# Performance work log

Measured on AMD Instinct MI355X. Metric: run time of the kernel, lower is better.

The kernel has to match this reference:

```python
import jax, jax.numpy as jnp
import numpy as np

NUM_HEADS = 12


def _get_rel_pos(q_size, k_size, rel_pos):
    # q_size == k_size here, so the torch interpolate branch is never taken;
    # table already has 2*max(q,k)-1 rows. Gather by relative coordinate.
    coords = jnp.arange(q_size)[:, None] - jnp.arange(k_size)[None, :] + (k_size - 1)
    return rel_pos[coords]  # (q_size, k_size, head_dim)


def setup_inputs() -> dict:
    key = jax.random.key(0)
    ks = jax.random.split(key, 8)
    B, D, H, W, dim = 32, 8, 8, 8, 768
    hd = dim // NUM_HEADS
    s = 0.02
    return {
        "x": jax.random.normal(ks[0], (B, D, H, W, dim), jnp.float32),
        "w_qkv": jax.random.normal(ks[1], (dim, 3 * dim), jnp.float32) * s,
        "b_qkv": jnp.zeros((3 * dim,), jnp.float32),
        "w_proj": jax.random.normal(ks[2], (dim, dim), jnp.float32) * s,
        "b_proj": jnp.zeros((dim,), jnp.float32),
        "rel_pos_d": jax.random.normal(ks[3], (2 * D - 1, hd), jnp.float32) * s,
        "rel_pos_h": jax.random.normal(ks[4], (2 * H - 1, hd), jnp.float32) * s,
        "rel_pos_w": jax.random.normal(ks[5], (2 * W - 1, hd), jnp.float32) * s,
    }


def reference(x, w_qkv, b_qkv, w_proj, b_proj, rel_pos_d, rel_pos_h, rel_pos_w):
    B, D, H, W, dim = x.shape
    nH = NUM_HEADS
    hd = dim // nH
    N = D * H * W
    scale = hd ** -0.5

    # qkv projection: (B, N, 3, nH, hd) -> (3, B*nH, N, hd)
    qkv = (x.reshape(B, N, dim) @ w_qkv + b_qkv).reshape(B, N, 3, nH, hd)
    qkv = jnp.transpose(qkv, (2, 0, 3, 1, 4)).reshape(3, B * nH, N, hd)
    q, k, v = qkv[0], qkv[1], qkv[2]

    attn = jnp.einsum('bqc,bkc->bqk', q * scale, k)  # (B*nH, N, N)

    # decomposed relative positional bias (MViTv2-style)
    Rd = _get_rel_pos(D, D, rel_pos_d)  # (D, D, hd)
    Rh = _get_rel_pos(H, H, rel_pos_h)  # (H, H, hd)
    Rw = _get_rel_pos(W, W, rel_pos_w)  # (W, W, hd)
    r_q = q.reshape(B * nH, D, H, W, hd)
    rel_d = jnp.einsum('bdhwc,dkc->bdhwk', r_q, Rd)
    rel_h = jnp.einsum('bdhwc,hkc->bdhwk', r_q, Rh)
    rel_w = jnp.einsum('bdhwc,wkc->bdhwk', r_q, Rw)

    attn = attn.reshape(B * nH, D, H, W, D, H, W)
    attn = (attn
            + rel_d[:, :, :, :, :, None, None]
            + rel_h[:, :, :, :, None, :, None]
            + rel_w[:, :, :, :, None, None, :])
    attn = jax.nn.softmax(attn.reshape(B * nH, N, N), axis=-1)

    out = (attn @ v).reshape(B, nH, D, H, W, hd)
    out = jnp.transpose(out, (0, 2, 3, 4, 1, 5)).reshape(B, D, H, W, dim)
    return out @ w_proj + b_proj
```

## Files before the change

### kernel.cpp

```cpp
#include <hip/hip_runtime.h>
#include <hip/hip_bf16.h>
#include <cstdint>

typedef __bf16 bf16x8 __attribute__((ext_vector_type(8)));
typedef __bf16 bf16x4 __attribute__((ext_vector_type(4)));
typedef float  f32x4  __attribute__((ext_vector_type(4)));
typedef float  f32x16 __attribute__((ext_vector_type(16)));
typedef unsigned u32x4 __attribute__((ext_vector_type(4)));

__device__ __forceinline__ f32x4 mfma16(bf16x8 a, bf16x8 b, f32x4 c) {
  return __builtin_amdgcn_mfma_f32_16x16x32_bf16(a, b, c, 0, 0, 0);
}
__device__ __forceinline__ f32x16 mfma32(bf16x8 a, bf16x8 b, f32x16 c) {
  return __builtin_amdgcn_mfma_f32_32x32x16_bf16(a, b, c, 0, 0, 0);
}

__device__ __forceinline__ void gload_lds16(const __bf16* g, __bf16* l) {
  __builtin_amdgcn_global_load_lds(
      (const __attribute__((address_space(1))) void*)g,
      (__attribute__((address_space(3))) void*)l, 16, 0, 0);
}

__device__ __forceinline__ unsigned cvtpk(float lo, float hi) {
  unsigned r;
  asm("v_cvt_pk_bf16_f32 %0, %1, %2" : "=v"(r) : "v"(lo), "v"(hi));
  return r;
}
__device__ __forceinline__ void plswap(unsigned& a, unsigned& b) {
  asm("v_permlane32_swap_b32 %0, %1" : "+v"(a), "+v"(b));
}

__global__ __launch_bounds__(256) void cvt_bf16_kernel(const float* __restrict__ in,
                                                       __bf16* __restrict__ out, int n4) {
  int i = blockIdx.x * 256 + threadIdx.x;
  if (i < n4) {
    float4 v = ((const float4*)in)[i];
    bf16x4 o;
    o[0] = (__bf16)v.x; o[1] = (__bf16)v.y; o[2] = (__bf16)v.z; o[3] = (__bf16)v.w;
    ((bf16x4*)out)[i] = o;
  }
}

__global__ __launch_bounds__(256) void transpose_cvt_kernel(const float* __restrict__ src,
                                                            __bf16* __restrict__ dst,
                                                            int R, int C) {
  __shared__ float tile[32][33];
  int r0 = blockIdx.y * 32, c0 = blockIdx.x * 32;
  int tx = threadIdx.x & 31, ty = threadIdx.x >> 5;
#pragma unroll
  for (int i = 0; i < 4; ++i)
    tile[ty + i * 8][tx] = src[(size_t)(r0 + ty + i * 8) * C + c0 + tx];
  __syncthreads();
#pragma unroll
  for (int i = 0; i < 4; ++i) {
    int rr = ty + i * 8;
    dst[(size_t)(c0 + rr) * R + r0 + tx] = (__bf16)tile[tx][rr];
  }
}

template <int EPI>
__global__ __launch_bounds__(256) void gemm_bt_kernel(
    const __bf16* __restrict__ A, const __bf16* __restrict__ Bt,
    int M, int N, int K, int nbx,
    const float* __restrict__ bias,
    float* __restrict__ outF,
    __bf16* __restrict__ qo, __bf16* __restrict__ ko, __bf16* __restrict__ vTo) {
  __shared__ __attribute__((aligned(16))) __bf16 lds[2][2][4096];
  const int t = threadIdx.x;
  const int l = t & 63, w = t >> 6;
  const int wm = (w >> 1) * 64, wn = (w & 1) * 64;
  const int cpx = gridDim.x >> 3;
  const int wg = (blockIdx.x & 7) * cpx + (blockIdx.x >> 3);
  const int m0 = (wg / nbx) * 128, n0 = (wg % nbx) * 128;
  const int nk = K >> 5;

  auto stage = [&](int buf, int kt) {
    const __bf16* As = A + (size_t)m0 * K + kt * 32;
    const __bf16* Bs = Bt + (size_t)n0 * K + kt * 32;
#pragma unroll
    for (int rnd = 0; rnd < 2; ++rnd) {
      int li = rnd * 256 + t;
      int row = li >> 2, c8 = (li & 3) * 8;
      gload_lds16(As + (size_t)row * K + c8, &lds[buf][0][li * 8]);
      gload_lds16(Bs + (size_t)row * K + c8, &lds[buf][1][li * 8]);
    }
  };

  f32x4 acc[4][4] = {};
  stage(0, 0);
  __syncthreads();
  int buf = 0;
  for (int kt = 0; kt < nk; ++kt) {
    if (kt + 1 < nk) stage(buf ^ 1, kt + 1);
    bf16x8 af[4], bfv[4];
    const __bf16* la = &lds[buf][0][0];
    const __bf16* lb = &lds[buf][1][0];
#pragma unroll
    for (int mt = 0; mt < 4; ++mt)
      af[mt] = *(const bf16x8*)(la + (wm + mt * 16 + (l & 15)) * 32 + (l >> 4) * 8);
#pragma unroll
    for (int nt = 0; nt < 4; ++nt)
      bfv[nt] = *(const bf16x8*)(lb + (wn + nt * 16 + (l & 15)) * 32 + (l >> 4) * 8);
#pragma unroll
    for (int mt = 0; mt < 4; ++mt)
#pragma unroll
      for (int nt = 0; nt < 4; ++nt)
        acc[mt][nt] = mfma16(af[mt], bfv[nt], acc[mt][nt]);
    __syncthreads();
    buf ^= 1;
  }

#pragma unroll
  for (int mt = 0; mt < 4; ++mt) {
#pragma unroll
    for (int nt = 0; nt < 4; ++nt) {
#pragma unroll
      for (int r = 0; r < 4; ++r) {
        int row = m0 + wm + mt * 16 + (l >> 4) * 4 + r;
        int col = n0 + wn + nt * 16 + (l & 15);
        float val = acc[mt][nt][r] + bias[col];
        if constexpr (EPI == 0) {
          int s = col / 768, rem = col - s * 768;
          int h = rem >> 6, c = rem & 63;
          int b = row >> 9, n = row & 511;
          size_t bh = (size_t)(b * 12 + h);
          __bf16 bv = (__bf16)val;
          if (s == 0)      qo[(bh * 512 + n) * 64 + c] = bv;
          else if (s == 1) ko[(bh * 512 + n) * 64 + c] = bv;
          else             vTo[(bh * 64 + c) * 512 + n] = bv;
        } else {
          outF[(size_t)row * N + col] = val;
        }
      }
    }
  }
}

__device__ __forceinline__ const bf16x8* kfrag(const __bf16* base, int row, int ch) {
  return (const bf16x8*)(base + row * 64 + ((ch ^ (row & 7)) * 8));
}
__device__ __forceinline__ const bf16x8* vfrag(const __bf16* base, int row, int ch) {
  return (const bf16x8*)(base + row * 32 + ((ch ^ ((row >> 1) & 3)) * 8));
}

__global__ __launch_bounds__(256, 4) void attn_kernel(
    const __bf16* __restrict__ qg_, const __bf16* __restrict__ kg,
    const __bf16* __restrict__ vT,
    const float* __restrict__ rpd, const float* __restrict__ rph,
    const float* __restrict__ rpw,
    __bf16* __restrict__ attn_out) {
  const int bid = (blockIdx.x & 7) * 192 + (blockIdx.x >> 3);
  const int bh = bid >> 2;
  const int qb = bid & 3;
  const int t = threadIdx.x, w = t >> 6, l = t & 63;
  const int lq = l & 31, lh5 = l >> 5;

  __shared__ float bias_lds[128][25];
  __shared__ float rs_lds[4][32];
  __shared__ __attribute__((aligned(16))) __bf16 k_lds[2][32 * 64];
  __shared__ __attribute__((aligned(16))) __bf16 v_lds[2][64 * 32];

  const __bf16* kb = kg + (size_t)bh * 512 * 64;
  const __bf16* vb = vT + (size_t)bh * 64 * 512;

  auto stage = [&](int sbuf, int j0) {
    {
      int row = t >> 3, pc = t & 7;
      int lc = pc ^ (row & 7);
      gload_lds16(kb + (size_t)(j0 + row) * 64 + lc * 8, &k_lds[sbuf][t * 8]);
    }
    {
      int row = t >> 2, pc = t & 3;
      int lc = pc ^ ((row >> 1) & 3);
      gload_lds16(vb + (size_t)row * 512 + j0 + lc * 8, &v_lds[sbuf][t * 8]);
    }
  };

  stage(0, 0);

  const __bf16* qbase = qg_ + ((size_t)bh * 512 + qb * 128 + w * 32) * 64;
  bf16x8 qf[4];
#pragma unroll
  for (int s = 0; s < 4; ++s)
    qf[s] = *(const bf16x8*)(qbase + lq * 64 + s * 16 + lh5 * 8);

  {
    const int row = w * 32 + lq;
    const int n = qb * 128 + row;
    const int dd = n >> 6, hh = (n >> 3) & 7, ww = n & 7;
#pragma unroll
    for (int jt = 0; jt < 2; ++jt) {
      const float* src;
      if (jt == 0) src = (lq < 15) ? rpd + (size_t)lq * 64
                                   : (lq >= 16 && lq < 31) ? rph + (size_t)(lq - 16) * 64
                                                           : nullptr;
      else         src = (lq < 15) ? rpw + (size_t)lq * 64 : nullptr;
      f32x16 cb = {};
#pragma unroll
      for (int s = 0; s < 4; ++s) {
        bf16x8 afr;
        if (src) {
          float4 a = *(const float4*)(src + s * 16 + lh5 * 8);
          float4 b = *(const float4*)(src + s * 16 + lh5 * 8 + 4);
          u32x4 u = {cvtpk(a.x, a.y), cvtpk(a.z, a.w), cvtpk(b.x, b.y), cvtpk(b.z, b.w)};
          afr = __builtin_bit_cast(bf16x8, u);
        } else {
          afr = bf16x8{};
        }
        cb = mfma32(afr, qf[s], cb);
      }
#pragma unroll
      for (int r = 0; r < 16; ++r) {
        int j = (r & 3) + 8 * (r >> 2) + 4 * lh5;
        if (jt == 0) {
          if (j < 16) {
            int idx = dd + 7 - j;
            if (idx >= 0 && idx < 8) bias_lds[row][idx] = cb[r];
          } else {
            int idx = hh + 7 - (j - 16);
            if (idx >= 0 && idx < 8) bias_lds[row][8 + idx] = cb[r];
          }
        } else {
          if (j < 16) {
            int idx = ww + 7 - j;
            if (idx >= 0 && idx < 8) bias_lds[row][16 + idx] = cb[r];
          }
        }
      }
    }
  }

  __syncthreads();

  const float LOG2E = 1.44269504f;
  const float* brow = &bias_lds[w * 32 + lq][0];
  float bh2e[4], bh2o[4], bw2[4];
#pragma unroll
  for (int rr = 0; rr < 4; ++rr) {
    bh2e[rr] = brow[8 + rr] * LOG2E;
    bh2o[rr] = brow[12 + rr] * LOG2E;
    bw2[rr] = brow[16 + rr + 4 * lh5] * LOG2E;
  }

  f32x16 accO0 = {}, accO1 = {};
  float rs4[4] = {0.f, 0.f, 0.f, 0.f};
  const float scale2 = 0.125f * LOG2E;

  for (int kk = 0; kk < 8; ++kk) {
#pragma unroll
    for (int par = 0; par < 2; ++par) {
      const int kb_i = kk * 2 + par;
      if (kb_i < 15) stage(par ^ 1, (kb_i + 1) * 32);
      const __bf16* kl = k_lds[par];
      const __bf16* vl = v_lds[par];

      f32x16 accS = {};
#pragma unroll
      for (int s = 0; s < 4; ++s)
        accS = mfma32(*kfrag(kl, lq, lh5 + 2 * s), qf[s], accS);

      float bd2 = brow[kb_i >> 1] * LOG2E;
      float pr[16];
#pragma unroll
      for (int rr = 0; rr < 4; ++rr) {
        float bsum = bd2 + (par ? bh2o[rr] : bh2e[rr]);
#pragma unroll
        for (int c = 0; c < 4; ++c) {
          int r = rr * 4 + c;
          float p = __builtin_amdgcn_exp2f(accS[r] * scale2 + bsum + bw2[c]);
          rs4[rr] += p;
          pr[r] = p;
        }
      }

      unsigned a0 = cvtpk(pr[0], pr[1]),   b0 = cvtpk(pr[4], pr[5]);
      unsigned a1 = cvtpk(pr[2], pr[3]),   b1 = cvtpk(pr[6], pr[7]);
      unsigned a2 = cvtpk(pr[8], pr[9]),   b2 = cvtpk(pr[12], pr[13]);
      unsigned a3 = cvtpk(pr[10], pr[11]), b3 = cvtpk(pr[14], pr[15]);
      plswap(a0, b0); plswap(a1, b1); plswap(a2, b2); plswap(a3, b3);
      u32x4 u0 = {a0, a1, b0, b1};
      u32x4 u1 = {a2, a3, b2, b3};
      bf16x8 pf0 = __builtin_bit_cast(bf16x8, u0);
      bf16x8 pf1 = __builtin_bit_cast(bf16x8, u1);

      accO0 = mfma32(pf0, *vfrag(vl, lq, lh5), accO0);
      accO0 = mfma32(pf1, *vfrag(vl, lq, lh5 + 2), accO0);
      accO1 = mfma32(pf0, *vfrag(vl, 32 + lq, lh5), accO1);
      accO1 = mfma32(pf1, *vfrag(vl, 32 + lq, lh5 + 2), accO1);

      __syncthreads();
    }
  }

  {
    float rsum = (rs4[0] + rs4[1]) + (rs4[2] + rs4[3]);
    float s = rsum + __shfl_xor(rsum, 32);
    if (l < 32) rs_lds[w][l] = 1.f / s;
  }

  const int b_ = bh / 12, h_ = bh - b_ * 12;
  __bf16* obase = attn_out + ((size_t)b_ * 512 + qb * 128 + w * 32) * 768 + h_ * 64;
#pragma unroll
  for (int rr = 0; rr < 4; ++rr) {
#pragma unroll
    for (int c = 0; c < 4; ++c) {
      int r = rr * 4 + c;
      int qrow = c + 8 * rr + 4 * lh5;
      float inv = rs_lds[w][qrow];
      obase[(size_t)qrow * 768 + lq]      = (__bf16)(accO0[r] * inv);
      obase[(size_t)qrow * 768 + 32 + lq] = (__bf16)(accO1[r] * inv);
    }
  }
}

extern "C" void kernel_launch(void* const* d_in, const int* in_sizes, int n_in,
                              void* d_out, int out_size, void* d_ws, size_t ws_size,
                              hipStream_t stream) {
  const float* x      = (const float*)d_in[0];
  const float* w_qkv  = (const float*)d_in[1];
  const float* b_qkv  = (const float*)d_in[2];
  const float* w_proj = (const float*)d_in[3];
  const float* b_proj = (const float*)d_in[4];
  const float* rpd    = (const float*)d_in[5];
  const float* rph    = (const float*)d_in[6];
  const float* rpw    = (const float*)d_in[7];
  float* out = (float*)d_out;

  char* base = (char*)d_ws;
  __bf16* xb     = (__bf16*)(base);
  __bf16* wqkvT  = (__bf16*)(base + 25165824);
  __bf16* wprojT = (__bf16*)(base + 25165824 + 3538944);
  __bf16* qb     = (__bf16*)(base + 25165824 + 3538944 + 1179648);
  __bf16* kb     = qb + (size_t)384 * 512 * 64;
  __bf16* vT     = kb + (size_t)384 * 512 * 64;

  cvt_bf16_kernel<<<12288, 256, 0, stream>>>(x, xb, 12582912 / 4);
  transpose_cvt_kernel<<<dim3(2304 / 32, 768 / 32), 256, 0, stream>>>(w_qkv, wqkvT, 768, 2304);
  transpose_cvt_kernel<<<dim3(768 / 32, 768 / 32), 256, 0, stream>>>(w_proj, wprojT, 768, 768);

  gemm_bt_kernel<0><<<2304, 256, 0, stream>>>(
      xb, wqkvT, 16384, 2304, 768, 18, b_qkv, nullptr, qb, kb, vT);

  attn_kernel<<<1536, 256, 0, stream>>>(qb, kb, vT, rpd, rph, rpw, xb);

  gemm_bt_kernel<1><<<768, 256, 0, stream>>>(
      xb, wprojT, 16384, 768, 768, 6, b_proj, out, nullptr, nullptr, nullptr);
}
```

Measured before the change: 200.1 us.

## Use 256x128 GEMM tiles with 512 threads and deeper prefetch pipeline

The bf16 GEMM now uses 8 waves (512 threads) per block over a 256x128 output tile, so each B tile loaded into LDS is reused across twice as many rows. The single-stage prefetch plus __syncthreads is replaced by two stages in flight, explicit s_waitcnt vmcnt(3), raw s_barrier and sched_barrier fences. This aims to hide global-to-LDS latency and cut B-operand traffic. In exchange it relies on hand-tuned wait counts and issues redundant loads on the last iterations, and it halves the block count, which risks load imbalance.

After: 205.2 us. 2.6% more time.

```diff
diff --git a/kernel.cpp b/kernel.cpp
--- a/kernel.cpp
+++ b/kernel.cpp
@@ -59,19 +59,20 @@
 }
 
 template <int EPI>
-__global__ __launch_bounds__(256) void gemm_bt_kernel(
+__global__ __launch_bounds__(512) void gemm_bt2_kernel(
     const __bf16* __restrict__ A, const __bf16* __restrict__ Bt,
     int M, int N, int K, int nbx,
     const float* __restrict__ bias,
     float* __restrict__ outF,
     __bf16* __restrict__ qo, __bf16* __restrict__ ko, __bf16* __restrict__ vTo) {
-  __shared__ __attribute__((aligned(16))) __bf16 lds[2][2][4096];
+  __shared__ __attribute__((aligned(16))) __bf16 lA[2][256 * 32];
+  __shared__ __attribute__((aligned(16))) __bf16 lB[2][128 * 32];
   const int t = threadIdx.x;
   const int l = t & 63, w = t >> 6;
   const int wm = (w >> 1) * 64, wn = (w & 1) * 64;
   const int cpx = gridDim.x >> 3;
   const int wg = (blockIdx.x & 7) * cpx + (blockIdx.x >> 3);
-  const int m0 = (wg / nbx) * 128, n0 = (wg % nbx) * 128;
+  const int m0 = (wg / nbx) * 256, n0 = (wg % nbx) * 128;
   const int nk = K >> 5;
 
   auto stage = [&](int buf, int kt) {
@@ -79,22 +80,27 @@
     const __bf16* Bs = Bt + (size_t)n0 * K + kt * 32;
 #pragma unroll
     for (int rnd = 0; rnd < 2; ++rnd) {
-      int li = rnd * 256 + t;
+      int li = rnd * 512 + t;
       int row = li >> 2, c8 = (li & 3) * 8;
-      gload_lds16(As + (size_t)row * K + c8, &lds[buf][0][li * 8]);
-      gload_lds16(Bs + (size_t)row * K + c8, &lds[buf][1][li * 8]);
+      gload_lds16(As + (size_t)row * K + c8, &lA[buf][li * 8]);
+    }
+    {
+      int row = t >> 2, c8 = (t & 3) * 8;
+      gload_lds16(Bs + (size_t)row * K + c8, &lB[buf][t * 8]);
     }
   };
 
   f32x4 acc[4][4] = {};
   stage(0, 0);
-  __syncthreads();
-  int buf = 0;
+  stage(1, 1);
+
   for (int kt = 0; kt < nk; ++kt) {
-    if (kt + 1 < nk) stage(buf ^ 1, kt + 1);
+    asm volatile("s_waitcnt vmcnt(3)" ::: "memory");
+    __builtin_amdgcn_s_barrier();
+    __builtin_amdgcn_sched_barrier(0);
+    const __bf16* la = &lA[kt & 1][0];
+    const __bf16* lb = &lB[kt & 1][0];
     bf16x8 af[4], bfv[4];
-    const __bf16* la = &lds[buf][0][0];
-    const __bf16* lb = &lds[buf][1][0];
 #pragma unroll
     for (int mt = 0; mt < 4; ++mt)
       af[mt] = *(const bf16x8*)(la + (wm + mt * 16 + (l & 15)) * 32 + (l >> 4) * 8);
@@ -106,8 +112,11 @@
 #pragma unroll
       for (int nt = 0; nt < 4; ++nt)
         acc[mt][nt] = mfma16(af[mt], bfv[nt], acc[mt][nt]);
-    __syncthreads();
-    buf ^= 1;
+    __builtin_amdgcn_sched_barrier(0);
+    __builtin_amdgcn_s_barrier();
+    __builtin_amdgcn_sched_barrier(0);
+    int nxt = kt + 2 < nk ? kt + 2 : nk - 1;
+    stage(kt & 1, nxt);
   }
 
 #pragma unroll
@@ -338,11 +347,11 @@
   transpose_cvt_kernel<<<dim3(2304 / 32, 768 / 32), 256, 0, stream>>>(w_qkv, wqkvT, 768, 2304);
   transpose_cvt_kernel<<<dim3(768 / 32, 768 / 32), 256, 0, stream>>>(w_proj, wprojT, 768, 768);
 
-  gemm_bt_kernel<0><<<2304, 256, 0, stream>>>(
+  gemm_bt2_kernel<0><<<1152, 512, 0, stream>>>(
       xb, wqkvT, 16384, 2304, 768, 18, b_qkv, nullptr, qb, kb, vT);
 
   attn_kernel<<<1536, 256, 0, stream>>>(qb, kb, vT, rpd, rph, rpw, xb);
 
-  gemm_bt_kernel<1><<<768, 256, 0, stream>>>(
+  gemm_bt2_kernel<1><<<384, 512, 0, stream>>>(
       xb, wprojT, 16384, 768, 768, 6, b_proj, out, nullptr, nullptr, nullptr);
 }
```
